# Optimization experiments

Hardware: AMD Instinct MI355X
Metric: run time of the kernel (lower is better)

The kernel has to match this reference:

```python
import jax, jax.numpy as jnp
import numpy as np

N_NODES = 100000
N_EDGES = 1600000
NUM_FEATURES = 128
NUM_CLASSES = 10
NUM_GRAPHS = 64


def setup_inputs() -> dict:
    key = jax.random.key(0)
    ks = jax.random.split(key, 16)
    x = jax.random.normal(ks[0], (N_NODES, NUM_FEATURES), dtype=jnp.float32)
    edge_index = jax.random.randint(ks[1], (2, N_EDGES), 0, N_NODES, dtype=jnp.int64)
    batch = jnp.sort(jax.random.randint(ks[2], (N_NODES,), 0, NUM_GRAPHS, dtype=jnp.int64))

    def glorot(k, fan_in, fan_out):
        s = jnp.sqrt(6.0 / (fan_in + fan_out)).astype(jnp.float32)
        return jax.random.uniform(k, (fan_in, fan_out), jnp.float32, -s, s)

    dims = [(NUM_FEATURES, 128), (128, 128), (128, 128), (128, 64), (64, 32)]
    params = {}
    for i, (fi, fo) in enumerate(dims, start=1):
        params[f"W{i}"] = glorot(ks[2 + i], fi, fo)
        params[f"b{i}"] = jnp.zeros((fo,), jnp.float32)
    params["Wfc"] = glorot(ks[10], 32, NUM_CLASSES)
    params["bfc"] = jnp.zeros((NUM_CLASSES,), jnp.float32)
    return {"x": x, "edge_index": edge_index, "batch": batch, **params}


def reference(x, edge_index, batch, W1, b1, W2, b2, W3, b3, W4, b4, W5, b5, Wfc, bfc):
    N = x.shape[0]
    loops = jnp.arange(N, dtype=edge_index.dtype)
    src = jnp.concatenate([edge_index[0], loops])  # message source j
    dst = jnp.concatenate([edge_index[1], loops])  # message target i
    # GCN symmetric normalization: deg computed on targets incl. self loops
    deg = jax.ops.segment_sum(jnp.ones_like(dst, x.dtype), dst, num_segments=N)
    dinv = jnp.where(deg > 0, jax.lax.rsqrt(deg), 0.0)
    norm = (dinv[src] * dinv[dst])[:, None]  # [E+N, 1]

    def gcn_conv(h, W, b):
        h = h @ W  # transform first (smaller gather width when out < in)
        msg = h[src] * norm
        return jax.ops.segment_sum(msg, dst, num_segments=N) + b

    h = jax.nn.relu(gcn_conv(x, W1, b1))
    h = jax.nn.relu(gcn_conv(h, W2, b2))
    h = jax.nn.relu(gcn_conv(h, W3, b3))
    h = jax.nn.relu(gcn_conv(h, W4, b4))
    h = jax.nn.relu(gcn_conv(h, W5, b5))

    # global_mean_pool over graph membership
    sums = jax.ops.segment_sum(h, batch, num_segments=NUM_GRAPHS)
    cnts = jax.ops.segment_sum(jnp.ones((N,), h.dtype), batch, num_segments=NUM_GRAPHS)
    pooled = sums / jnp.maximum(cnts, 1.0)[:, None]

    # dropout is identity in eval mode
    return pooled @ Wfc + bfc
```

## Files before the change

### kernel.cpp

```cpp
#include <hip/hip_runtime.h>
#include <hip/hip_bf16.h>

#define N_NODES 100000
#define N_EDGES 1600000
#define N_GRAPHS 64
#define WNB 192
#define BCAP 64

typedef __attribute__((ext_vector_type(8))) short bf16x8;
typedef __attribute__((ext_vector_type(4))) float f32x4;

__device__ inline float bflo(unsigned u) { return __uint_as_float(u << 16); }
__device__ inline float bfhi(unsigned u) { return __uint_as_float(u & 0xffff0000u); }
__device__ inline unsigned short f2bf(float f) {
    unsigned u = __float_as_uint(f);
    return (unsigned short)((u + 0x7fff + ((u >> 16) & 1)) >> 16);
}


__global__ __launch_bounds__(256) void k_curinit(int* __restrict__ cursor, int n) {
    int i = blockIdx.x * 256 + threadIdx.x;
    if (i < n) cursor[i] = i * BCAP;
}

__global__ __launch_bounds__(256) void k_fillw(const int* __restrict__ ei,
                                               int* __restrict__ cursor,
                                               int* __restrict__ cols, int e) {
    const int w = blockIdx.x & 7;
    const int b = blockIdx.x >> 3;
    const int lo = w * 12500, hi = lo + 12500;
    const int4* s4 = (const int4*)ei;
    const int4* d4 = (const int4*)(ei + e);
    const int n4 = e >> 2;
    for (int i = b * 256 + threadIdx.x; i < n4; i += WNB * 256) {
        int4 d = d4[i];
        int4 s = s4[i];
        if (d.x >= lo && d.x < hi) {
            int p = atomicAdd(&cursor[d.x], 1);
            if (p < d.x * BCAP + BCAP) cols[p] = s.x;
        }
        if (d.y >= lo && d.y < hi) {
            int p = atomicAdd(&cursor[d.y], 1);
            if (p < d.y * BCAP + BCAP) cols[p] = s.y;
        }
        if (d.z >= lo && d.z < hi) {
            int p = atomicAdd(&cursor[d.z], 1);
            if (p < d.z * BCAP + BCAP) cols[p] = s.z;
        }
        if (d.w >= lo && d.w < hi) {
            int p = atomicAdd(&cursor[d.w], 1);
            if (p < d.w * BCAP + BCAP) cols[p] = s.w;
        }
    }
}

__global__ __launch_bounds__(256) void k_dinv(const int* __restrict__ cursor,
                                              float* __restrict__ dinv, int n) {
    int i = blockIdx.x * 256 + threadIdx.x;
    if (i < n) dinv[i] = rsqrtf((float)(cursor[i] - BCAP * i + 1));
}


__global__ __launch_bounds__(256) void k_wconv5(const float* __restrict__ W1,
                                                const float* __restrict__ W2,
                                                const float* __restrict__ W3,
                                                const float* __restrict__ W4,
                                                const float* __restrict__ W5,
                                                unsigned short* __restrict__ wt1,
                                                unsigned short* __restrict__ wt2,
                                                unsigned short* __restrict__ wt3,
                                                unsigned short* __restrict__ wt4,
                                                unsigned short* __restrict__ wt5) {
    int i = blockIdx.x * 256 + threadIdx.x;
    const float* W; unsigned short* WT; int FI, FO, j;
    if (i < 16384)      { W = W1; WT = wt1; FI = 128; FO = 128; j = i; }
    else if (i < 32768) { W = W2; WT = wt2; FI = 128; FO = 128; j = i - 16384; }
    else if (i < 49152) { W = W3; WT = wt3; FI = 128; FO = 128; j = i - 32768; }
    else if (i < 57344) { W = W4; WT = wt4; FI = 128; FO = 64;  j = i - 49152; }
    else if (i < 59392) { W = W5; WT = wt5; FI = 64;  FO = 32;  j = i - 57344; }
    else return;
    int n_ = j / FI, k_ = j % FI;
    WT[j] = f2bf(W[(size_t)k_ * FO + n_]);
}


template <int FI, int FO, bool AF32>
__global__ __launch_bounds__(256) void k_gemm(const void* __restrict__ Ain,
                                              const unsigned short* __restrict__ WT,
                                              unsigned short* __restrict__ Tout, int n) {
    constexpr int NT = FO / 16;
    constexpr int NC = FI / 32;
    const int wave = threadIdx.x >> 6;
    const int lane = threadIdx.x & 63;
    const int m = lane & 15;
    const int q = lane >> 4;
    const int row0 = blockIdx.x * 64 + wave * 16;
    int arow = row0 + m;
    if (arow > n - 1) arow = n - 1;

    f32x4 acc[NT];
    #pragma unroll
    for (int j = 0; j < NT; j++) acc[j] = (f32x4){0.f, 0.f, 0.f, 0.f};

    #pragma unroll
    for (int c = 0; c < NC; c++) {
        const int k0 = c * 32 + q * 8;
        bf16x8 a;
        if constexpr (AF32) {
            const float* ap = (const float*)Ain + (size_t)arow * FI + k0;
            float4 f0 = *reinterpret_cast<const float4*>(ap);
            float4 f1 = *reinterpret_cast<const float4*>(ap + 4);
            a[0] = (short)f2bf(f0.x); a[1] = (short)f2bf(f0.y);
            a[2] = (short)f2bf(f0.z); a[3] = (short)f2bf(f0.w);
            a[4] = (short)f2bf(f1.x); a[5] = (short)f2bf(f1.y);
            a[6] = (short)f2bf(f1.z); a[7] = (short)f2bf(f1.w);
        } else {
            a = *reinterpret_cast<const bf16x8*>(
                    (const unsigned short*)Ain + (size_t)arow * FI + k0);
        }
        #pragma unroll
        for (int j = 0; j < NT; j++) {
            bf16x8 b = *reinterpret_cast<const bf16x8*>(
                           WT + (size_t)(j * 16 + m) * FI + k0);
            acc[j] = __builtin_amdgcn_mfma_f32_16x16x32_bf16(a, b, acc[j], 0, 0, 0);
        }
    }

    #pragma unroll
    for (int r = 0; r < 4; r++) {
        int row = row0 + q * 4 + r;
        if (row < n) {
            #pragma unroll
            for (int j = 0; j < NT; j++)
                Tout[(size_t)row * FO + j * 16 + m] = f2bf(acc[j][r]);
        }
    }
}


template <int FO, int UNR>
__global__ __launch_bounds__(256) void k_agg(const unsigned short* __restrict__ T,
                                             const int* __restrict__ cursor,
                                             const int* __restrict__ cols,
                                             const float* __restrict__ dinv,
                                             const float* __restrict__ bias,
                                             unsigned short* __restrict__ Hout, int n) {
    constexpr int LPE = FO / 8;
    constexpr int EPW = 64 / LPE;
    int node = blockIdx.x * 4 + (threadIdx.x >> 6);
    if (node >= n) return;
    node = __builtin_amdgcn_readfirstlane(node);
    const int lane = threadIdx.x & 63;
    const int sub = lane / LPE;
    const int li  = lane % LPE;

    const float dn = dinv[node];

    float acc[8];
    #pragma unroll
    for (int k = 0; k < 8; k++) acc[k] = 0.f;

    if (sub == 0) {
        float dii = dn * dn;
        uint4 u = reinterpret_cast<const uint4*>(T + (size_t)node * FO)[li];
        acc[0] = dii * bflo(u.x); acc[1] = dii * bfhi(u.x);
        acc[2] = dii * bflo(u.y); acc[3] = dii * bfhi(u.y);
        acc[4] = dii * bflo(u.z); acc[5] = dii * bfhi(u.z);
        acc[6] = dii * bflo(u.w); acc[7] = dii * bfhi(u.w);
    }

    const int e0 = node * BCAP;
    int e1 = cursor[node];
    if (e1 > e0 + BCAP) e1 = e0 + BCAP;
    int e = e0 + sub;
    for (; e + (UNR - 1) * EPW < e1; e += UNR * EPW) {
        int cs[UNR]; float ws[UNR]; uint4 tv[UNR];
        #pragma unroll
        for (int u = 0; u < UNR; u++)
            cs[u] = __builtin_nontemporal_load(&cols[e + u * EPW]);
        #pragma unroll
        for (int u = 0; u < UNR; u++)
            tv[u] = reinterpret_cast<const uint4*>(T + (size_t)cs[u] * FO)[li];
        #pragma unroll
        for (int u = 0; u < UNR; u++)
            ws[u] = dinv[cs[u]] * dn;
        #pragma unroll
        for (int u = 0; u < UNR; u++) {
            float w = ws[u];
            acc[0] += w * bflo(tv[u].x); acc[1] += w * bfhi(tv[u].x);
            acc[2] += w * bflo(tv[u].y); acc[3] += w * bfhi(tv[u].y);
            acc[4] += w * bflo(tv[u].z); acc[5] += w * bfhi(tv[u].z);
            acc[6] += w * bflo(tv[u].w); acc[7] += w * bfhi(tv[u].w);
        }
    }
    for (; e < e1; e += EPW) {
        int c = __builtin_nontemporal_load(&cols[e]);
        uint4 tv = reinterpret_cast<const uint4*>(T + (size_t)c * FO)[li];
        float w = dinv[c] * dn;
        acc[0] += w * bflo(tv.x); acc[1] += w * bfhi(tv.x);
        acc[2] += w * bflo(tv.y); acc[3] += w * bfhi(tv.y);
        acc[4] += w * bflo(tv.z); acc[5] += w * bfhi(tv.z);
        acc[6] += w * bflo(tv.w); acc[7] += w * bfhi(tv.w);
    }

    #pragma unroll
    for (int off = LPE; off < 64; off <<= 1) {
        #pragma unroll
        for (int k = 0; k < 8; k++) acc[k] += __shfl_xor(acc[k], off);
    }

    if (sub == 0) {
        float4 ba = reinterpret_cast<const float4*>(bias)[2 * li];
        float4 bb = reinterpret_cast<const float4*>(bias)[2 * li + 1];
        float r0 = fmaxf(acc[0] + ba.x, 0.f);
        float r1 = fmaxf(acc[1] + ba.y, 0.f);
        float r2 = fmaxf(acc[2] + ba.z, 0.f);
        float r3 = fmaxf(acc[3] + ba.w, 0.f);
        float r4 = fmaxf(acc[4] + bb.x, 0.f);
        float r5 = fmaxf(acc[5] + bb.y, 0.f);
        float r6 = fmaxf(acc[6] + bb.z, 0.f);
        float r7 = fmaxf(acc[7] + bb.w, 0.f);
        uint4 pk;
        pk.x = (unsigned)f2bf(r0) | ((unsigned)f2bf(r1) << 16);
        pk.y = (unsigned)f2bf(r2) | ((unsigned)f2bf(r3) << 16);
        pk.z = (unsigned)f2bf(r4) | ((unsigned)f2bf(r5) << 16);
        pk.w = (unsigned)f2bf(r6) | ((unsigned)f2bf(r7) << 16);
        reinterpret_cast<uint4*>(Hout + (size_t)node * FO)[li] = pk;
    }
}


__global__ __launch_bounds__(256) void k_pool2(const unsigned short* __restrict__ H,
                                               const int* __restrict__ batch,
                                               float* __restrict__ pooled, int n) {
    __shared__ float red0[256], red1[256];
    __shared__ int se[2];
    int g = blockIdx.x;
    int t = threadIdx.x;
    if (t < 2) {
        int target = g + t;
        int lo = 0, hi = n;
        while (lo < hi) {
            int mid = (lo + hi) >> 1;
            if (batch[mid] < target) lo = mid + 1; else hi = mid;
        }
        se[t] = lo;
    }
    __syncthreads();
    int s = se[0], e = se[1];
    int c = t & 15;
    int grp = t >> 4;
    float a0 = 0.f, a1 = 0.f;
    for (int i = s + grp; i < e; i += 16) {
        unsigned u = reinterpret_cast<const unsigned*>(H + (size_t)i * 32)[c];
        a0 += bflo(u); a1 += bfhi(u);
    }
    red0[t] = a0; red1[t] = a1;
    __syncthreads();
    for (int off = 128; off >= 16; off >>= 1) {
        if (t < off) { red0[t] += red0[t + off]; red1[t] += red1[t + off]; }
        __syncthreads();
    }
    if (t < 16) {
        float cnt = fmaxf((float)(e - s), 1.0f);
        pooled[g * 32 + 2 * t]     = red0[t] / cnt;
        pooled[g * 32 + 2 * t + 1] = red1[t] / cnt;
    }
}

__global__ __launch_bounds__(256) void k_fc(const float* __restrict__ pooled,
                                            const float* __restrict__ Wfc,
                                            const float* __restrict__ bfc,
                                            float* __restrict__ out) {
    __shared__ float pl[N_GRAPHS * 32];
    int t = threadIdx.x;
    for (int m = t; m < N_GRAPHS * 32; m += 256) pl[m] = pooled[m];
    __syncthreads();
    for (int o = t; o < N_GRAPHS * 10; o += 256) {
        int g = o / 10, c = o % 10;
        float a = bfc[c];
        #pragma unroll
        for (int k = 0; k < 32; k++) a += pl[g * 32 + k] * Wfc[k * 10 + c];
        out[o] = a;
    }
}


extern "C" void kernel_launch(void* const* d_in, const int* in_sizes, int n_in,
                              void* d_out, int out_size, void* d_ws, size_t ws_size,
                              hipStream_t stream) {
    const int N = N_NODES, E = N_EDGES;

    const float* x     = (const float*)d_in[0];
    const int*   ei    = (const int*)d_in[1];
    const int*   batch = (const int*)d_in[2];
    const float* W1 = (const float*)d_in[3];  const float* b1 = (const float*)d_in[4];
    const float* W2 = (const float*)d_in[5];  const float* b2 = (const float*)d_in[6];
    const float* W3 = (const float*)d_in[7];  const float* b3 = (const float*)d_in[8];
    const float* W4 = (const float*)d_in[9];  const float* b4 = (const float*)d_in[10];
    const float* W5 = (const float*)d_in[11]; const float* b5 = (const float*)d_in[12];
    const float* Wfc = (const float*)d_in[13]; const float* bfc = (const float*)d_in[14];
    float* out = (float*)d_out;

    char* p = (char*)d_ws;
    auto take = [&](size_t b) { char* q = p; p += (b + 511) & ~(size_t)511; return q; };
    int*   cursor = (int*)take((size_t)N * 4);
    float* dinv   = (float*)take((size_t)N * 4);
    float* pooled = (float*)take(N_GRAPHS * 32 * 4);
    int*   cols   = (int*)take((size_t)N * BCAP * 4);
    unsigned short* wt1 = (unsigned short*)take(128 * 128 * 2);
    unsigned short* wt2 = (unsigned short*)take(128 * 128 * 2);
    unsigned short* wt3 = (unsigned short*)take(128 * 128 * 2);
    unsigned short* wt4 = (unsigned short*)take(128 * 64 * 2);
    unsigned short* wt5 = (unsigned short*)take(64 * 32 * 2);
    unsigned short* T   = (unsigned short*)take((size_t)N * 128 * 2);
    unsigned short* H   = (unsigned short*)take((size_t)N * 128 * 2);

    const int nb = (N + 255) / 256;

    k_curinit<<<nb, 256, 0, stream>>>(cursor, N);
    k_fillw<<<8 * WNB, 256, 0, stream>>>(ei, cursor, cols, E);
    k_dinv<<<nb, 256, 0, stream>>>(cursor, dinv, N);

    k_wconv5<<<232, 256, 0, stream>>>(W1, W2, W3, W4, W5, wt1, wt2, wt3, wt4, wt5);

    const int gemmb = (N + 63) / 64;
    const int aggb  = (N + 3) / 4;

    k_gemm<128, 128, true ><<<gemmb, 256, 0, stream>>>(x, wt1, T, N);
    k_agg<128, 4><<<aggb, 256, 0, stream>>>(T, cursor, cols, dinv, b1, H, N);

    k_gemm<128, 128, false><<<gemmb, 256, 0, stream>>>(H, wt2, T, N);
    k_agg<128, 4><<<aggb, 256, 0, stream>>>(T, cursor, cols, dinv, b2, H, N);

    k_gemm<128, 128, false><<<gemmb, 256, 0, stream>>>(H, wt3, T, N);
    k_agg<128, 4><<<aggb, 256, 0, stream>>>(T, cursor, cols, dinv, b3, H, N);

    k_gemm<128, 64, false><<<gemmb, 256, 0, stream>>>(H, wt4, T, N);
    k_agg<64, 2><<<aggb, 256, 0, stream>>>(T, cursor, cols, dinv, b4, H, N);

    k_gemm<64, 32, false><<<gemmb, 256, 0, stream>>>(H, wt5, T, N);
    k_agg<32, 1><<<aggb, 256, 0, stream>>>(T, cursor, cols, dinv, b5, H, N);

    k_pool2<<<N_GRAPHS, 256, 0, stream>>>(H, batch, pooled, N);
    k_fc<<<1, 256, 0, stream>>>(pooled, Wfc, bfc, out);
}
```

Measured before the change: 669.0 us.

## Store 128-wide features in feature-sliced layout and aggregate per slice

```diff
diff --git a/kernel.cpp b/kernel.cpp
--- a/kernel.cpp
+++ b/kernel.cpp
@@ -84,7 +84,7 @@
 }
 
 
-template <int FI, int FO, bool AF32>
+template <int FI, int FO, bool AF32, bool ASM, bool OSM>
 __global__ __launch_bounds__(256) void k_gemm(const void* __restrict__ Ain,
                                               const unsigned short* __restrict__ WT,
                                               unsigned short* __restrict__ Tout, int n) {
@@ -114,6 +114,10 @@
             a[2] = (short)f2bf(f0.z); a[3] = (short)f2bf(f0.w);
             a[4] = (short)f2bf(f1.x); a[5] = (short)f2bf(f1.y);
             a[6] = (short)f2bf(f1.z); a[7] = (short)f2bf(f1.w);
+        } else if constexpr (ASM) {
+            a = *reinterpret_cast<const bf16x8*>(
+                    (const unsigned short*)Ain +
+                    ((size_t)(k0 >> 4) * N_NODES + arow) * 16 + (k0 & 15));
         } else {
             a = *reinterpret_cast<const bf16x8*>(
                     (const unsigned short*)Ain + (size_t)arow * FI + k0);
@@ -131,9 +135,84 @@
         int row = row0 + q * 4 + r;
         if (row < n) {
             #pragma unroll
-            for (int j = 0; j < NT; j++)
-                Tout[(size_t)row * FO + j * 16 + m] = f2bf(acc[j][r]);
-        }
+            for (int j = 0; j < NT; j++) {
+                if constexpr (OSM)
+                    Tout[((size_t)j * N_NODES + row) * 16 + m] = f2bf(acc[j][r]);
+                else
+                    Tout[(size_t)row * FO + j * 16 + m] = f2bf(acc[j][r]);
+            }
+        }
+    }
+}
+
+
+__global__ __launch_bounds__(256) void k_aggs(const unsigned short* __restrict__ T_s,
+                                              const int* __restrict__ cursor,
+                                              const int* __restrict__ cols,
+                                              const float* __restrict__ dinv,
+                                              const float* __restrict__ bias,
+                                              unsigned short* __restrict__ H_s, int n) {
+    const int s = blockIdx.x & 7;
+    int node = (blockIdx.x >> 3) * 4 + (threadIdx.x >> 6);
+    if (node >= n) return;
+    node = __builtin_amdgcn_readfirstlane(node);
+    const int lane = threadIdx.x & 63;
+    const int sub = lane >> 1;
+    const int li  = lane & 1;
+    const unsigned short* Ts = T_s + (size_t)s * N_NODES * 16;
+
+    const float dn = dinv[node];
+
+    float acc[8];
+    #pragma unroll
+    for (int k = 0; k < 8; k++) acc[k] = 0.f;
+
+    if (sub == 0) {
+        float dii = dn * dn;
+        uint4 u = reinterpret_cast<const uint4*>(Ts + (size_t)node * 16)[li];
+        acc[0] = dii * bflo(u.x); acc[1] = dii * bfhi(u.x);
+        acc[2] = dii * bflo(u.y); acc[3] = dii * bfhi(u.y);
+        acc[4] = dii * bflo(u.z); acc[5] = dii * bfhi(u.z);
+        acc[6] = dii * bflo(u.w); acc[7] = dii * bfhi(u.w);
+    }
+
+    const int e0 = node * BCAP;
+    int e1 = cursor[node];
+    if (e1 > e0 + BCAP) e1 = e0 + BCAP;
+    for (int e = e0 + sub; e < e1; e += 32) {
+        int c = __builtin_nontemporal_load(&cols[e]);
+        uint4 tv = reinterpret_cast<const uint4*>(Ts + (size_t)c * 16)[li];
+        float w = dinv[c] * dn;
+        acc[0] += w * bflo(tv.x); acc[1] += w * bfhi(tv.x);
+        acc[2] += w * bflo(tv.y); acc[3] += w * bfhi(tv.y);
+        acc[4] += w * bflo(tv.z); acc[5] += w * bfhi(tv.z);
+        acc[6] += w * bflo(tv.w); acc[7] += w * bfhi(tv.w);
+    }
+
+    #pragma unroll
+    for (int off = 2; off < 64; off <<= 1) {
+        #pragma unroll
+        for (int k = 0; k < 8; k++) acc[k] += __shfl_xor(acc[k], off);
+    }
+
+    if (sub == 0) {
+        const float* bp = bias + s * 16 + li * 8;
+        float4 ba = reinterpret_cast<const float4*>(bp)[0];
+        float4 bb = reinterpret_cast<const float4*>(bp)[1];
+        float r0 = fmaxf(acc[0] + ba.x, 0.f);
+        float r1 = fmaxf(acc[1] + ba.y, 0.f);
+        float r2 = fmaxf(acc[2] + ba.z, 0.f);
+        float r3 = fmaxf(acc[3] + ba.w, 0.f);
+        float r4 = fmaxf(acc[4] + bb.x, 0.f);
+        float r5 = fmaxf(acc[5] + bb.y, 0.f);
+        float r6 = fmaxf(acc[6] + bb.z, 0.f);
+        float r7 = fmaxf(acc[7] + bb.w, 0.f);
+        uint4 pk;
+        pk.x = (unsigned)f2bf(r0) | ((unsigned)f2bf(r1) << 16);
+        pk.y = (unsigned)f2bf(r2) | ((unsigned)f2bf(r3) << 16);
+        pk.z = (unsigned)f2bf(r4) | ((unsigned)f2bf(r5) << 16);
+        pk.w = (unsigned)f2bf(r6) | ((unsigned)f2bf(r7) << 16);
+        reinterpret_cast<uint4*>(H_s + ((size_t)s * N_NODES + node) * 16)[li] = pk;
     }
 }
 
@@ -313,8 +392,8 @@
     unsigned short* wt3 = (unsigned short*)take(128 * 128 * 2);
     unsigned short* wt4 = (unsigned short*)take(128 * 64 * 2);
     unsigned short* wt5 = (unsigned short*)take(64 * 32 * 2);
-    unsigned short* T   = (unsigned short*)take((size_t)N * 128 * 2);
-    unsigned short* H   = (unsigned short*)take((size_t)N * 128 * 2);
+    unsigned short* Ta  = (unsigned short*)take((size_t)N * 128 * 2);
+    unsigned short* Hs  = (unsigned short*)take((size_t)N * 128 * 2);
 
     const int nb = (N + 255) / 256;
 
@@ -326,22 +405,23 @@
 
     const int gemmb = (N + 63) / 64;
     const int aggb  = (N + 3) / 4;
-
-    k_gemm<128, 128, true ><<<gemmb, 256, 0, stream>>>(x, wt1, T, N);
-    k_agg<128, 4><<<aggb, 256, 0, stream>>>(T, cursor, cols, dinv, b1, H, N);
-
-    k_gemm<128, 128, false><<<gemmb, 256, 0, stream>>>(H, wt2, T, N);
-    k_agg<128, 4><<<aggb, 256, 0, stream>>>(T, cursor, cols, dinv, b2, H, N);
-
-    k_gemm<128, 128, false><<<gemmb, 256, 0, stream>>>(H, wt3, T, N);
-    k_agg<128, 4><<<aggb, 256, 0, stream>>>(T, cursor, cols, dinv, b3, H, N);
-
-    k_gemm<128, 64, false><<<gemmb, 256, 0, stream>>>(H, wt4, T, N);
-    k_agg<64, 2><<<aggb, 256, 0, stream>>>(T, cursor, cols, dinv, b4, H, N);
-
-    k_gemm<64, 32, false><<<gemmb, 256, 0, stream>>>(H, wt5, T, N);
-    k_agg<32, 1><<<aggb, 256, 0, stream>>>(T, cursor, cols, dinv, b5, H, N);
-
-    k_pool2<<<N_GRAPHS, 256, 0, stream>>>(H, batch, pooled, N);
+    const int aggsb = 8 * aggb;
+
+    k_gemm<128, 128, true,  false, true ><<<gemmb, 256, 0, stream>>>(x, wt1, Ta, N);
+    k_aggs<<<aggsb, 256, 0, stream>>>(Ta, cursor, cols, dinv, b1, Hs, N);
+
+    k_gemm<128, 128, false, true,  true ><<<gemmb, 256, 0, stream>>>(Hs, wt2, Ta, N);
+    k_aggs<<<aggsb, 256, 0, stream>>>(Ta, cursor, cols, dinv, b2, Hs, N);
+
+    k_gemm<128, 128, false, true,  true ><<<gemmb, 256, 0, stream>>>(Hs, wt3, Ta, N);
+    k_aggs<<<aggsb, 256, 0, stream>>>(Ta, cursor, cols, dinv, b3, Hs, N);
+
+    k_gemm<128, 64, false, true,  false><<<gemmb, 256, 0, stream>>>(Hs, wt4, Ta, N);
+    k_agg<64, 2><<<aggb, 256, 0, stream>>>(Ta, cursor, cols, dinv, b4, Hs, N);
+
+    k_gemm<64, 32, false, false, false><<<gemmb, 256, 0, stream>>>(Hs, wt5, Ta, N);
+    k_agg<32, 1><<<aggb, 256, 0, stream>>>(Ta, cursor, cols, dinv, b5, Hs, N);
+
+    k_pool2<<<N_GRAPHS, 256, 0, stream>>>(Hs, batch, pooled, N);
     k_fc<<<1, 256, 0, stream>>>(pooled, Wfc, bfc, out);
 }
```

Result: slower. 1.424 ms (+112.8%).
